# Kernel tuning notes

Measured on AMD Instinct MI355X. Metric: run time of the kernel, lower is better.

The kernel has to match this reference:

```python
import jax, jax.numpy as jnp
import numpy as np

NUM_SLOTS = 4096
NUM_CLUSTER = 10
SLOT_DIM = 64
EPS = 1e-8
N_ITER = 3
LN_EPS = 1e-5


def _ln(x, g, b):
    m = jnp.mean(x, axis=-1, keepdims=True)
    v = jnp.var(x, axis=-1, keepdims=True)
    return (x - m) / jnp.sqrt(v + LN_EPS) * g + b


def setup_inputs() -> dict:
    key = jax.random.key(0)
    ks = jax.random.split(key, 24)
    d, S = SLOT_DIM, NUM_SLOTS
    s = d ** -0.5
    f32 = jnp.float32
    return {
        "cluster_centers": jax.random.normal(ks[0], (NUM_CLUSTER, d), f32),
        "Wk": jax.random.normal(ks[1], (d, d), f32) * s,
        "bk": jnp.zeros((d,), f32),
        "Wq": jax.random.normal(ks[2], (d, d), f32) * s,
        "bq": jnp.zeros((d,), f32),
        "Wv": jax.random.normal(ks[3], (d, d), f32) * s,
        "bv": jnp.zeros((d,), f32),
        "cc_g": jnp.ones((d,), f32),
        "cc_b": jnp.zeros((d,), f32),
        "W_ih": jax.random.normal(ks[4], (3 * d, d), f32) * s,
        "W_hh": jax.random.normal(ks[5], (3 * d, d), f32) * s,
        "b_ih": jnp.zeros((3 * d,), f32),
        "b_hh": jnp.zeros((3 * d,), f32),
        "ln_g": jnp.ones((d,), f32),
        "ln_b": jnp.zeros((d,), f32),
        "W1": jax.random.normal(ks[6], (2 * d, d), f32) * s,
        "b1": jnp.zeros((2 * d,), f32),
        "W2": jax.random.normal(ks[7], (d, 2 * d), f32) * (2 * d) ** -0.5,
        "b2": jnp.zeros((d,), f32),
        "Wa": jax.random.normal(ks[8], (S, d, d), f32) * s,
        "ba": jnp.zeros((S, d), f32),
        "Wb": jax.random.normal(ks[9], (S, d, d), f32) * s,
        "bb": jnp.zeros((S, d), f32),
    }


def reference(cluster_centers, Wk, bk, Wq, bq, Wv, bv, cc_g, cc_b,
              W_ih, W_hh, b_ih, b_hh, ln_g, ln_b, W1, b1, W2, b2,
              Wa, ba, Wb, bb):
    temp = SLOT_DIM ** -0.5
    k = cluster_centers @ Wk.T + bk          # [N, d]
    v = cluster_centers @ Wv.T + bv          # [N, d]
    cc = cluster_centers
    for _ in range(N_ITER):
        cc_prev = cc
        q = _ln(cc, cc_g, cc_b) @ Wq.T + bq  # [N, d]
        attn = jnp.einsum('nd,md->nm', k, q) * temp
        attn = jax.nn.softmax(attn, axis=0) + EPS
        attn = attn / jnp.sum(attn, axis=-1, keepdims=True)
        updates = attn @ v                   # [N, d]
        # PyTorch GRUCell
        gi = updates @ W_ih.T + b_ih
        gh = cc_prev @ W_hh.T + b_hh
        ir, iz, inn = jnp.split(gi, 3, axis=-1)
        hr, hz, hn = jnp.split(gh, 3, axis=-1)
        r = jax.nn.sigmoid(ir + hr)
        z = jax.nn.sigmoid(iz + hz)
        n = jnp.tanh(inn + r * hn)
        cc = (1.0 - z) * n + z * cc_prev
        # residual MLP
        h = _ln(cc, ln_g, ln_b)
        cc = cc + jax.nn.relu(h @ W1.T + b1) @ W2.T + b2
    # per-slot 2-layer MLP + max over the 10 clusters, vectorized over slots
    h = jax.nn.relu(jnp.einsum('sij,nj->sni', Wa, cc) + ba[:, None, :])  # [S, N, d]
    out = jnp.einsum('sij,snj->sni', Wb, h) + bb[:, None, :]             # [S, N, d]
    return jnp.max(out, axis=1)                                          # [S, d]
```

## Files before the change

kernel.cpp:

```cpp
#include <hip/hip_runtime.h>
#include <math.h>

#define NCLU 10
#define D    64
#define NSLOT 4096

typedef unsigned int   u32;
typedef unsigned short u16;

typedef __attribute__((ext_vector_type(8))) short  bf16x8;
typedef __attribute__((ext_vector_type(4))) float  f32x4;

__device__ __forceinline__ u16 f2bf_rne(float f) {
    u32 u = __float_as_uint(f);
    return (u16)((u + 0x7fffu + ((u >> 16) & 1u)) >> 16);
}

__device__ __forceinline__ bf16x8 pack8(float4 a, float4 b) {
    bf16x8 r;
    r[0] = (short)f2bf_rne(a.x); r[1] = (short)f2bf_rne(a.y);
    r[2] = (short)f2bf_rne(a.z); r[3] = (short)f2bf_rne(a.w);
    r[4] = (short)f2bf_rne(b.x); r[5] = (short)f2bf_rne(b.y);
    r[6] = (short)f2bf_rne(b.z); r[7] = (short)f2bf_rne(b.w);
    return r;
}

__device__ __forceinline__ float wred(float v) {
#pragma unroll
    for (int off = 32; off > 0; off >>= 1) v += __shfl_xor(v, off);
    return v;
}

__device__ __forceinline__ void load_afrags64(bf16x8 a[4][2], const float* __restrict__ W,
                                              int lc, int quad) {
#pragma unroll
    for (int mt = 0; mt < 4; ++mt)
#pragma unroll
        for (int kt = 0; kt < 2; ++kt) {
            const float* p = W + (16 * mt + lc) * 64 + kt * 32 + quad * 8;
            a[mt][kt] = pack8(*(const float4*)p, *(const float4*)(p + 4));
        }
}

__device__ __forceinline__ void load_afrags128(bf16x8 a[4][2], const float* __restrict__ W,
                                               int ktbase, int lc, int quad) {
#pragma unroll
    for (int mt = 0; mt < 4; ++mt)
#pragma unroll
        for (int kt = 0; kt < 2; ++kt) {
            const float* p = W + (16 * mt + lc) * 128 + (ktbase + kt) * 32 + quad * 8;
            a[mt][kt] = pack8(*(const float4*)p, *(const float4*)(p + 4));
        }
}

__device__ __forceinline__ bf16x8 bfrag(const float* __restrict__ xbase, int xstride,
                                        int lc, int quad, int ktglob) {
    if (lc < NCLU) {
        const float* p = xbase + lc * xstride + ktglob * 32 + quad * 8;
        return pack8(*(const float4*)p, *(const float4*)(p + 4));
    }
    bf16x8 z;
#pragma unroll
    for (int j = 0; j < 8; ++j) z[j] = 0;
    return z;
}

__device__ __forceinline__ void mm_apply(const bf16x8 a[4][2], const float* __restrict__ xbase,
                                         int xstride, int ktbase,
                                         float* __restrict__ obase, int ostride, int ooff,
                                         const float* __restrict__ bias, bool do_relu,
                                         int lc, int quad) {
    f32x4 acc[4];
#pragma unroll
    for (int mt = 0; mt < 4; ++mt) acc[mt] = (f32x4){0.f, 0.f, 0.f, 0.f};
#pragma unroll
    for (int kt = 0; kt < 2; ++kt) {
        bf16x8 b = bfrag(xbase, xstride, lc, quad, ktbase + kt);
#pragma unroll
        for (int mt = 0; mt < 4; ++mt)
            acc[mt] = __builtin_amdgcn_mfma_f32_16x16x32_bf16(a[mt][kt], b, acc[mt], 0, 0, 0);
    }
    if (lc < NCLU) {
#pragma unroll
        for (int mt = 0; mt < 4; ++mt) {
            float4 o;
            o.x = acc[mt][0]; o.y = acc[mt][1]; o.z = acc[mt][2]; o.w = acc[mt][3];
            if (bias) {
                float4 bv = *(const float4*)(bias + 16 * mt + 4 * quad);
                o.x += bv.x; o.y += bv.y; o.z += bv.z; o.w += bv.w;
            }
            if (do_relu) {
                o.x = fmaxf(o.x, 0.f); o.y = fmaxf(o.y, 0.f);
                o.z = fmaxf(o.z, 0.f); o.w = fmaxf(o.w, 0.f);
            }
            *(float4*)(obase + lc * ostride + ooff + 16 * mt + 4 * quad) = o;
        }
    }
}

__global__ __launch_bounds__(640, 3) void phase1_kernel(
    const float* __restrict__ cc0,
    const float* __restrict__ Wk, const float* __restrict__ bk,
    const float* __restrict__ Wq, const float* __restrict__ bq,
    const float* __restrict__ Wv, const float* __restrict__ bv,
    const float* __restrict__ cc_g, const float* __restrict__ cc_b,
    const float* __restrict__ W_ih, const float* __restrict__ W_hh,
    const float* __restrict__ b_ih, const float* __restrict__ b_hh,
    const float* __restrict__ ln_g, const float* __restrict__ ln_b,
    const float* __restrict__ W1, const float* __restrict__ b1,
    const float* __restrict__ W2, const float* __restrict__ b2,
    float* __restrict__ cc_out)
{
    const int t = threadIdx.x;
    const int w = t >> 6;
    const int i = t & 63;
    const int quad = i >> 4;
    const int lc   = i & 15;

    __shared__ float ccl[NCLU][68];
    __shared__ float xl[NCLU][68];
    __shared__ float kl[NCLU][68];
    __shared__ float vl[NCLU][68];
    __shared__ float ql[NCLU][68];
    __shared__ float ul[NCLU][68];
    __shared__ float hl[NCLU][68];
    __shared__ float dl9[NCLU][68];
    __shared__ float dl8[NCLU][68];
    __shared__ float tl[NCLU][132];
    __shared__ float gl[6][NCLU][68];
    __shared__ float al[NCLU][12];

    const float g_cc = cc_g[i], b_cc = cc_b[i];
    const float g_ln = ln_g[i], b_ln = ln_b[i];

    bf16x8 afrA[4][2], afrB[4][2];
#pragma unroll
    for (int mt = 0; mt < 4; ++mt)
#pragma unroll
        for (int kt = 0; kt < 2; ++kt) {
#pragma unroll
            for (int j = 0; j < 8; ++j) { afrA[mt][kt][j] = 0; afrB[mt][kt][j] = 0; }
        }

    const float* biasA = nullptr;
    if (w == 0)      { load_afrags64(afrA, Wq, lc, quad);                    biasA = bq; }
    else if (w <= 3) { load_afrags64(afrA, W_ih + (w - 1) * 64 * 64, lc, quad); biasA = b_ih + (w - 1) * 64; }
    else if (w <= 6) { load_afrags64(afrA, W_hh + (w - 4) * 64 * 64, lc, quad); biasA = b_hh + (w - 4) * 64; }
    else if (w == 7) { load_afrags64(afrA, Wk, lc, quad); }
    else if (w == 8) { load_afrags64(afrA, Wv, lc, quad);
                       load_afrags128(afrB, W2, 2, lc, quad); }
    else             { load_afrags128(afrA, W2, 0, lc, quad); biasA = b2; }

    float c = cc0[w * 64 + i];
    ccl[w][i] = c;
    __syncthreads();

    if (w == 7)      mm_apply(afrA, &ccl[0][0], 68, 0, &kl[0][0], 68, 0, bk, false, lc, quad);
    else if (w == 8) mm_apply(afrA, &ccl[0][0], 68, 0, &vl[0][0], 68, 0, bv, false, lc, quad);
    __syncthreads();

    if (w == 7)      { load_afrags64(afrA, W1, lc, quad);            biasA = b1; }
    else if (w == 8) { load_afrags64(afrA, W1 + 64 * 64, lc, quad);  biasA = b1 + 64; }

    for (int it = 0; it < 3; ++it) {
        {
            float s1 = wred(c), s2 = wred(c * c);
            float mu = s1 * (1.f / 64.f);
            float va = s2 * (1.f / 64.f) - mu * mu;
            xl[w][i] = (c - mu) * rsqrtf(va + 1e-5f) * g_cc + b_cc;
        }
        __syncthreads();

        if (w == 0)
            mm_apply(afrA, &xl[0][0], 68, 0, &ql[0][0], 68, 0, biasA, false, lc, quad);
        else if (w >= 4 && w <= 6)
            mm_apply(afrA, &ccl[0][0], 68, 0, &gl[w - 1][0][0], 68, 0, biasA, false, lc, quad);
        __syncthreads();

        if (i < NCLU) {
            const float4* kf = (const float4*)&kl[w][0];
            const float4* qf = (const float4*)&ql[i][0];
            float a0 = 0.f, a1 = 0.f, a2 = 0.f, a3 = 0.f;
#pragma unroll
            for (int jj = 0; jj < 16; ++jj) {
                float4 kv = kf[jj], qv = qf[jj];
                a0 += kv.x * qv.x; a1 += kv.y * qv.y; a2 += kv.z * qv.z; a3 += kv.w * qv.w;
            }
            al[w][i] = ((a0 + a1) + (a2 + a3)) * 0.125f;
        }
        __syncthreads();

        if (t < NCLU) {
            float mx = -1e30f;
#pragma unroll
            for (int nn = 0; nn < NCLU; ++nn) mx = fmaxf(mx, al[nn][t]);
            float e[NCLU]; float s = 0.f;
#pragma unroll
            for (int nn = 0; nn < NCLU; ++nn) { e[nn] = __expf(al[nn][t] - mx); s += e[nn]; }
            float inv = 1.f / s;
#pragma unroll
            for (int nn = 0; nn < NCLU; ++nn) al[nn][t] = e[nn] * inv + 1e-8f;
        }
        __syncthreads();
        if (t < NCLU) {
            float s = 0.f;
#pragma unroll
            for (int m = 0; m < NCLU; ++m) s += al[t][m];
            float inv = 1.f / s;
#pragma unroll
            for (int m = 0; m < NCLU; ++m) al[t][m] *= inv;
        }
        __syncthreads();

        {
            float u = 0.f;
#pragma unroll
            for (int m = 0; m < NCLU; ++m) u += al[w][m] * vl[m][i];
            ul[w][i] = u;
        }
        __syncthreads();

        if (w >= 1 && w <= 3)
            mm_apply(afrA, &ul[0][0], 68, 0, &gl[w - 1][0][0], 68, 0, biasA, false, lc, quad);
        __syncthreads();

        {
            float ir = gl[0][w][i], iz = gl[1][w][i], inn = gl[2][w][i];
            float hr = gl[3][w][i], hz = gl[4][w][i], hn = gl[5][w][i];
            float r = 1.f / (1.f + __expf(-(ir + hr)));
            float z = 1.f / (1.f + __expf(-(iz + hz)));
            float nn2 = tanhf(inn + r * hn);
            c = (1.f - z) * nn2 + z * c;

            float s1 = wred(c), s2 = wred(c * c);
            float mu = s1 * (1.f / 64.f);
            float va = s2 * (1.f / 64.f) - mu * mu;
            hl[w][i] = (c - mu) * rsqrtf(va + 1e-5f) * g_ln + b_ln;
        }
        __syncthreads();

        if (w == 7)
            mm_apply(afrA, &hl[0][0], 68, 0, &tl[0][0], 132, 0, biasA, true, lc, quad);
        else if (w == 8)
            mm_apply(afrA, &hl[0][0], 68, 0, &tl[0][0], 132, 64, biasA, true, lc, quad);
        __syncthreads();

        if (w == 9)
            mm_apply(afrA, &tl[0][0], 132, 0, &dl9[0][0], 68, 0, biasA, false, lc, quad);
        else if (w == 8)
            mm_apply(afrB, &tl[0][0], 132, 2, &dl8[0][0], 68, 0, nullptr, false, lc, quad);
        __syncthreads();

        c += dl9[w][i] + dl8[w][i];
        ccl[w][i] = c;
        __syncthreads();
    }

    cc_out[w * 64 + i] = c;
}

#define WSTRIDE 72
__global__ __launch_bounds__(64, 4) void phase2_kernel(
    const float* __restrict__ Wa, const float* __restrict__ ba,
    const float* __restrict__ Wb, const float* __restrict__ bb,
    const float* __restrict__ cc, float* __restrict__ out)
{
    const int s = blockIdx.x;
    const int l = threadIdx.x;
    const int quad = l >> 4;
    const int lc   = l & 15;

    __shared__ u16 Wlds[64 * WSTRIDE];
    __shared__ u16 hT[16 * WSTRIDE];

    const float* wa = Wa + (size_t)s * 4096;
    const float* wb = Wb + (size_t)s * 4096;

    float4 rg[16];
#pragma unroll
    for (int cch = 0; cch < 16; ++cch)
        rg[cch] = *(const float4*)(wa + cch * 256 + l * 4);

    bf16x8 bfc[2];
#pragma unroll
    for (int kt = 0; kt < 2; ++kt) {
        if (lc < NCLU) {
            const float* cp = cc + lc * 64 + kt * 32 + quad * 8;
            bfc[kt] = pack8(*(const float4*)cp, *(const float4*)(cp + 4));
        } else {
#pragma unroll
            for (int j = 0; j < 8; ++j) bfc[kt][j] = 0;
        }
    }
    const float4 bav[4] = {
        *(const float4*)(ba + s * 64 + 0  + quad * 4),
        *(const float4*)(ba + s * 64 + 16 + quad * 4),
        *(const float4*)(ba + s * 64 + 32 + quad * 4),
        *(const float4*)(ba + s * 64 + 48 + quad * 4),
    };

#pragma unroll
    for (int cch = 0; cch < 16; ++cch) {
        int row = cch * 4 + quad;
        u32 p0 = (u32)f2bf_rne(rg[cch].x) | ((u32)f2bf_rne(rg[cch].y) << 16);
        u32 p1 = (u32)f2bf_rne(rg[cch].z) | ((u32)f2bf_rne(rg[cch].w) << 16);
        uint2 pk; pk.x = p0; pk.y = p1;
        *(uint2*)(&Wlds[row * WSTRIDE + lc * 4]) = pk;
    }

#pragma unroll
    for (int cch = 0; cch < 16; ++cch)
        rg[cch] = *(const float4*)(wb + cch * 256 + l * 4);

    f32x4 acc[4];
#pragma unroll
    for (int mt = 0; mt < 4; ++mt) acc[mt] = (f32x4){0.f, 0.f, 0.f, 0.f};
#pragma unroll
    for (int kt = 0; kt < 2; ++kt) {
#pragma unroll
        for (int mt = 0; mt < 4; ++mt) {
            bf16x8 af = *(const bf16x8*)(&Wlds[(16 * mt + lc) * WSTRIDE + kt * 32 + quad * 8]);
            acc[mt] = __builtin_amdgcn_mfma_f32_16x16x32_bf16(af, bfc[kt], acc[mt], 0, 0, 0);
        }
    }

#pragma unroll
    for (int mt = 0; mt < 4; ++mt) {
        u16 h0 = f2bf_rne(fmaxf(acc[mt][0] + bav[mt].x, 0.f));
        u16 h1 = f2bf_rne(fmaxf(acc[mt][1] + bav[mt].y, 0.f));
        u16 h2 = f2bf_rne(fmaxf(acc[mt][2] + bav[mt].z, 0.f));
        u16 h3 = f2bf_rne(fmaxf(acc[mt][3] + bav[mt].w, 0.f));
        uint2 pk; pk.x = (u32)h0 | ((u32)h1 << 16); pk.y = (u32)h2 | ((u32)h3 << 16);
        *(uint2*)(&hT[lc * WSTRIDE + 16 * mt + quad * 4]) = pk;
    }

#pragma unroll
    for (int cch = 0; cch < 16; ++cch) {
        int row = cch * 4 + quad;
        u32 p0 = (u32)f2bf_rne(rg[cch].x) | ((u32)f2bf_rne(rg[cch].y) << 16);
        u32 p1 = (u32)f2bf_rne(rg[cch].z) | ((u32)f2bf_rne(rg[cch].w) << 16);
        uint2 pk; pk.x = p0; pk.y = p1;
        *(uint2*)(&Wlds[row * WSTRIDE + lc * 4]) = pk;
    }

    f32x4 acc2[4];
#pragma unroll
    for (int mt = 0; mt < 4; ++mt) acc2[mt] = (f32x4){0.f, 0.f, 0.f, 0.f};
#pragma unroll
    for (int kt = 0; kt < 2; ++kt) {
        bf16x8 bf = *(const bf16x8*)(&hT[lc * WSTRIDE + kt * 32 + quad * 8]);
#pragma unroll
        for (int mt = 0; mt < 4; ++mt) {
            bf16x8 af = *(const bf16x8*)(&Wlds[(16 * mt + lc) * WSTRIDE + kt * 32 + quad * 8]);
            acc2[mt] = __builtin_amdgcn_mfma_f32_16x16x32_bf16(af, bf, acc2[mt], 0, 0, 0);
        }
    }

    const float NEG = -3.0e38f;
#pragma unroll
    for (int mt = 0; mt < 4; ++mt) {
#pragma unroll
        for (int r = 0; r < 4; ++r) {
            float v = (lc < NCLU) ? acc2[mt][r] : NEG;
#pragma unroll
            for (int off = 1; off < 16; off <<= 1)
                v = fmaxf(v, __shfl_xor(v, off));
            acc2[mt][r] = v;
        }
    }

    if (lc < 4) {
#pragma unroll
        for (int mt = 0; mt < 4; ++mt) {
            int row = 16 * mt + 4 * quad + lc;
            out[s * 64 + row] = acc2[mt][lc] + bb[s * 64 + row];
        }
    }
}

extern "C" void kernel_launch(void* const* d_in, const int* in_sizes, int n_in,
                              void* d_out, int out_size, void* d_ws, size_t ws_size,
                              hipStream_t stream) {
    const float* cc0  = (const float*)d_in[0];
    const float* Wk   = (const float*)d_in[1];
    const float* bk   = (const float*)d_in[2];
    const float* Wq   = (const float*)d_in[3];
    const float* bq   = (const float*)d_in[4];
    const float* Wv   = (const float*)d_in[5];
    const float* bv   = (const float*)d_in[6];
    const float* ccg  = (const float*)d_in[7];
    const float* ccb  = (const float*)d_in[8];
    const float* Wih  = (const float*)d_in[9];
    const float* Whh  = (const float*)d_in[10];
    const float* bih  = (const float*)d_in[11];
    const float* bhh  = (const float*)d_in[12];
    const float* lng  = (const float*)d_in[13];
    const float* lnb  = (const float*)d_in[14];
    const float* W1   = (const float*)d_in[15];
    const float* b1   = (const float*)d_in[16];
    const float* W2   = (const float*)d_in[17];
    const float* b2   = (const float*)d_in[18];
    const float* Wa   = (const float*)d_in[19];
    const float* ba   = (const float*)d_in[20];
    const float* Wb   = (const float*)d_in[21];
    const float* bb   = (const float*)d_in[22];

    float* cc_ws = (float*)d_ws;
    float* out   = (float*)d_out;

    hipLaunchKernelGGL(phase1_kernel, dim3(1), dim3(640), 0, stream,
                       cc0, Wk, bk, Wq, bq, Wv, bv, ccg, ccb,
                       Wih, Whh, bih, bhh, lng, lnb, W1, b1, W2, b2, cc_ws);

    hipLaunchKernelGGL(phase2_kernel, dim3(NSLOT), dim3(64), 0, stream,
                       Wa, ba, Wb, bb, cc_ws, out);
}
```

Measured before the change: 220.0 us.

## Stream Wa/Wb directly into LDS with global_load_lds and convert on read

Phase 2 now issues asynchronous direct global-to-LDS loads for both per-slot weight matrices at kernel start. This replaces the register staging, bf16 conversion and LDS store passes. The fp32 tiles are converted to bf16 when each MFMA operand is read from LDS, and a barrier is added before use. The aim is to overlap the Wb fetch with the first GEMM and cut VGPR pressure. In exchange, LDS per block grows to about 34KB of unpadded fp32 rows, which can cause bank conflicts and limit occupancy, and the launch-bounds occupancy hint is dropped.

```diff
diff --git a/kernel.cpp b/kernel.cpp
--- a/kernel.cpp
+++ b/kernel.cpp
@@ -259,8 +259,7 @@
     cc_out[w * 64 + i] = c;
 }
 
-#define WSTRIDE 72
-__global__ __launch_bounds__(64, 4) void phase2_kernel(
+__global__ __launch_bounds__(64) void phase2_kernel(
     const float* __restrict__ Wa, const float* __restrict__ ba,
     const float* __restrict__ Wb, const float* __restrict__ bb,
     const float* __restrict__ cc, float* __restrict__ out)
@@ -270,16 +269,25 @@
     const int quad = l >> 4;
     const int lc   = l & 15;
 
-    __shared__ u16 Wlds[64 * WSTRIDE];
-    __shared__ u16 hT[16 * WSTRIDE];
+    __shared__ float rawA[4096];
+    __shared__ float rawB[4096];
+    __shared__ u16   hT[16 * 72];
 
     const float* wa = Wa + (size_t)s * 4096;
     const float* wb = Wb + (size_t)s * 4096;
 
-    float4 rg[16];
-#pragma unroll
-    for (int cch = 0; cch < 16; ++cch)
-        rg[cch] = *(const float4*)(wa + cch * 256 + l * 4);
+#pragma unroll
+    for (int cch = 0; cch < 16; ++cch) {
+        __builtin_amdgcn_global_load_lds(
+            (const __attribute__((address_space(1))) void*)(wa + cch * 256 + l * 4),
+            (__attribute__((address_space(3))) void*)(&rawA[cch * 256]), 16, 0, 0);
+    }
+#pragma unroll
+    for (int cch = 0; cch < 16; ++cch) {
+        __builtin_amdgcn_global_load_lds(
+            (const __attribute__((address_space(1))) void*)(wb + cch * 256 + l * 4),
+            (__attribute__((address_space(3))) void*)(&rawB[cch * 256]), 16, 0, 0);
+    }
 
     bf16x8 bfc[2];
 #pragma unroll
@@ -299,18 +307,7 @@
         *(const float4*)(ba + s * 64 + 48 + quad * 4),
     };
 
-#pragma unroll
-    for (int cch = 0; cch < 16; ++cch) {
-        int row = cch * 4 + quad;
-        u32 p0 = (u32)f2bf_rne(rg[cch].x) | ((u32)f2bf_rne(rg[cch].y) << 16);
-        u32 p1 = (u32)f2bf_rne(rg[cch].z) | ((u32)f2bf_rne(rg[cch].w) << 16);
-        uint2 pk; pk.x = p0; pk.y = p1;
-        *(uint2*)(&Wlds[row * WSTRIDE + lc * 4]) = pk;
-    }
-
-#pragma unroll
-    for (int cch = 0; cch < 16; ++cch)
-        rg[cch] = *(const float4*)(wb + cch * 256 + l * 4);
+    __syncthreads();
 
     f32x4 acc[4];
 #pragma unroll
@@ -319,7 +316,8 @@
     for (int kt = 0; kt < 2; ++kt) {
 #pragma unroll
         for (int mt = 0; mt < 4; ++mt) {
-            bf16x8 af = *(const bf16x8*)(&Wlds[(16 * mt + lc) * WSTRIDE + kt * 32 + quad * 8]);
+            const float* p = &rawA[(16 * mt + lc) * 64 + kt * 32 + quad * 8];
+            bf16x8 af = pack8(*(const float4*)p, *(const float4*)(p + 4));
             acc[mt] = __builtin_amdgcn_mfma_f32_16x16x32_bf16(af, bfc[kt], acc[mt], 0, 0, 0);
         }
     }
@@ -331,27 +329,20 @@
         u16 h2 = f2bf_rne(fmaxf(acc[mt][2] + bav[mt].z, 0.f));
         u16 h3 = f2bf_rne(fmaxf(acc[mt][3] + bav[mt].w, 0.f));
         uint2 pk; pk.x = (u32)h0 | ((u32)h1 << 16); pk.y = (u32)h2 | ((u32)h3 << 16);
-        *(uint2*)(&hT[lc * WSTRIDE + 16 * mt + quad * 4]) = pk;
-    }
-
-#pragma unroll
-    for (int cch = 0; cch < 16; ++cch) {
-        int row = cch * 4 + quad;
-        u32 p0 = (u32)f2bf_rne(rg[cch].x) | ((u32)f2bf_rne(rg[cch].y) << 16);
-        u32 p1 = (u32)f2bf_rne(rg[cch].z) | ((u32)f2bf_rne(rg[cch].w) << 16);
-        uint2 pk; pk.x = p0; pk.y = p1;
-        *(uint2*)(&Wlds[row * WSTRIDE + lc * 4]) = pk;
-    }
+        *(uint2*)(&hT[lc * 72 + 16 * mt + quad * 4]) = pk;
+    }
+    __syncthreads();
 
     f32x4 acc2[4];
 #pragma unroll
     for (int mt = 0; mt < 4; ++mt) acc2[mt] = (f32x4){0.f, 0.f, 0.f, 0.f};
 #pragma unroll
     for (int kt = 0; kt < 2; ++kt) {
-        bf16x8 bf = *(const bf16x8*)(&hT[lc * WSTRIDE + kt * 32 + quad * 8]);
+        bf16x8 bf = *(const bf16x8*)(&hT[lc * 72 + kt * 32 + quad * 8]);
 #pragma unroll
         for (int mt = 0; mt < 4; ++mt) {
-            bf16x8 af = *(const bf16x8*)(&Wlds[(16 * mt + lc) * WSTRIDE + kt * 32 + quad * 8]);
+            const float* p = &rawB[(16 * mt + lc) * 64 + kt * 32 + quad * 8];
+            bf16x8 af = pack8(*(const float4*)p, *(const float4*)(p + 4));
             acc2[mt] = __builtin_amdgcn_mfma_f32_16x16x32_bf16(af, bf, acc2[mt], 0, 0, 0);
         }
     }
```

After: 226.0 us. 1.03x slower.
